# Optimization experiments

Measured on AMD Instinct MI355X. Metric: run time of the kernel, lower is better.

The kernel has to match this reference:

```python
import jax, jax.numpy as jnp
import numpy as np

K = 9      # kernel_size
H = 6      # num_head
HD = 64    # head_dim
D = H * HD # reduced_hidden_dim = 384
B, S = 16, 1024
OUT = 384  # hidden_dim // 2


def setup_inputs() -> dict:
    key = jax.random.key(0)
    k = jax.random.split(key, 5)
    q = jax.random.normal(k[0], (B, S, D), dtype=jnp.float32)
    ks = jax.random.normal(k[1], (B, S, D), dtype=jnp.float32)
    v = jax.random.normal(k[2], (B, S, D), dtype=jnp.float32)
    Wk = jax.random.normal(k[3], (K * H, D), dtype=jnp.float32) * 0.02
    bk = jnp.zeros((K * H,), dtype=jnp.float32)
    Wp = jax.random.normal(k[4], (OUT, D), dtype=jnp.float32) * 0.02
    bp = jnp.zeros((OUT,), dtype=jnp.float32)
    return {"q": q, "ks": ks, "v": v, "Wk": Wk, "bk": bk, "Wp": Wp, "bp": bp}


def reference(q, ks, v, Wk, bk, Wp, bp):
    b, s, d = v.shape
    pad = K // 2
    # expand4conv: zero-pad along seq and gather K-wide sliding windows
    vp = jnp.pad(v, ((0, 0), (pad, pad), (0, 0)))            # [B, S+K-1, D]
    win = jnp.stack([vp[:, i:i + s] for i in range(K)], -1)  # [B, S, D, K]
    win = win.reshape(b, s, H, HD, K)                        # [B, S, H, HD, K]
    # dynamic kernel: softmax over kernel taps
    logits = jnp.einsum('bsd,od->bso', q * ks, Wk) + bk       # [B, S, K*H]
    dk = jax.nn.softmax(logits.reshape(b, s, H, K), axis=-1)  # [B, S, H, K]
    # local weighted reduction over the window
    out = jnp.einsum('bshdk,bshk->bshd', win, dk).reshape(b, s, d)
    return jnp.einsum('bsd,od->bso', out, Wp) + bp            # [B, S, OUT]
```

## Files before the change

### kernel.cpp

```cpp
#include <hip/hip_runtime.h>
#include <hip/hip_bf16.h>

#define BB 16
#define SS 1024
#define DD 384
#define HH 6
#define HDD 64
#define KK 9
#define KH 54
#define NP 64
#define OUTD 384

typedef __attribute__((ext_vector_type(4))) float floatx4;
typedef __attribute__((ext_vector_type(8))) __bf16 bf16x8;
typedef __attribute__((ext_vector_type(4))) __bf16 bf16x4;

#define QLD 392
#define VLD 392

__global__ __launch_bounds__(256) void cast_kernel(const float* __restrict__ Wk,
                                                   const float* __restrict__ Wp,
                                                   __bf16* __restrict__ WkB,
                                                   __bf16* __restrict__ WpB) {
    int i = blockIdx.x * 256 + threadIdx.x;
    if (i < NP * DD) {
        int r = i / DD;
        WkB[i] = (r < KH) ? (__bf16)Wk[i] : (__bf16)0.0f;
    } else {
        int j = i - NP * DD;
        if (j < OUTD * DD) WpB[j] = (__bf16)Wp[j];
    }
}

__global__ __launch_bounds__(256) void fused_kernel(const float* __restrict__ q,
                                                    const float* __restrict__ ks,
                                                    const float* __restrict__ v,
                                                    const __bf16* __restrict__ WkB,
                                                    const float* __restrict__ bk,
                                                    __bf16* __restrict__ outA) {
    __shared__ __bf16 vqS[40 * VLD];
    __shared__ float  lgS[2 * 32 * 66];
    __shared__ float  dkS[32 * 56];

    const int tid  = threadIdx.x;
    const int wave = tid >> 6;
    const int lane = tid & 63;
    const int m0   = blockIdx.x * 32;
    const int b    = blockIdx.x >> 5;
    const int s0   = (blockIdx.x & 31) * 32;

    {
        const float* qb = q  + (size_t)m0 * DD;
        const float* kb = ks + (size_t)m0 * DD;
#pragma unroll
        for (int it = 0; it < 12; ++it) {
            int c = tid + it * 256;
            int row = c / 96, col = (c % 96) * 4;
            floatx4 qv = *reinterpret_cast<const floatx4*>(qb + (size_t)row * DD + col);
            floatx4 kv = *reinterpret_cast<const floatx4*>(kb + (size_t)row * DD + col);
            floatx4 pr = qv * kv;
            bf16x4 pk = { (__bf16)pr.x, (__bf16)pr.y, (__bf16)pr.z, (__bf16)pr.w };
            *reinterpret_cast<bf16x4*>(&vqS[row * VLD + col]) = pk;
        }
    }
    __syncthreads();

    {
        const int wm = (wave & 1) * 16;
        const int kh = wave >> 1;
        const int fr = lane & 15;
        const int fk = (lane >> 4) * 8;
        floatx4 acc[4] = {};
#pragma unroll
        for (int s = 0; s < 6; ++s) {
            int kk = kh * 192 + s * 32;
            bf16x8 afrag = *reinterpret_cast<const bf16x8*>(&vqS[(wm + fr) * VLD + kk + fk]);
#pragma unroll
            for (int j = 0; j < 4; ++j) {
                bf16x8 bfrag = *reinterpret_cast<const bf16x8*>(
                    WkB + (size_t)(j * 16 + fr) * DD + kk + fk);
                acc[j] = __builtin_amdgcn_mfma_f32_16x16x32_bf16(afrag, bfrag, acc[j], 0, 0, 0);
            }
        }
        const int col_in = lane & 15;
        const int rgrp   = (lane >> 4) * 4;
#pragma unroll
        for (int j = 0; j < 4; ++j)
#pragma unroll
            for (int r = 0; r < 4; ++r)
                lgS[(kh * 32 + wm + rgrp + r) * 66 + j * 16 + col_in] = acc[j][r];
    }
    __syncthreads();

    if (tid < 32 * HH) {
        int row = tid / HH, h = tid % HH;
        float lg[KK];
        float mx = -1e30f;
#pragma unroll
        for (int k = 0; k < KK; ++k) {
            int o = h * KK + k;
            float s = lgS[row * 66 + o] + lgS[(32 + row) * 66 + o] + bk[o];
            lg[k] = s;
            mx = fmaxf(mx, s);
        }
        float sum = 0.0f;
#pragma unroll
        for (int k = 0; k < KK; ++k) { lg[k] = __expf(lg[k] - mx); sum += lg[k]; }
        float inv = 1.0f / sum;
#pragma unroll
        for (int k = 0; k < KK; ++k) dkS[row * 56 + h * KK + k] = lg[k] * inv;
    }

    {
        const float* vb = v + (size_t)b * SS * DD;
#pragma unroll
        for (int it = 0; it < 15; ++it) {
            int c = tid + it * 256;
            int row = c / 96, col = (c % 96) * 4;
            int r = s0 + row - 4;
            floatx4 val = {};
            if (r >= 0 && r < SS)
                val = *reinterpret_cast<const floatx4*>(vb + (size_t)r * DD + col);
            bf16x4 vk = { (__bf16)val.x, (__bf16)val.y, (__bf16)val.z, (__bf16)val.w };
            *reinterpret_cast<bf16x4*>(&vqS[row * VLD + col]) = vk;
        }
    }
    __syncthreads();

    __bf16* ob = outA + (size_t)m0 * DD;
#pragma unroll
    for (int it = 0; it < 12; ++it) {
        int p = tid + it * 256;
        int row = p / 96, c4 = p % 96;
        int h = c4 >> 4;
        const float* dkr = &dkS[row * 56 + h * KK];
        floatx4 a = {};
#pragma unroll
        for (int k = 0; k < KK; ++k) {
            bf16x4 w = *reinterpret_cast<const bf16x4*>(&vqS[(row + k) * VLD + c4 * 4]);
            floatx4 wf = { (float)w[0], (float)w[1], (float)w[2], (float)w[3] };
            a += wf * dkr[k];
        }
        bf16x4 o = { (__bf16)a.x, (__bf16)a.y, (__bf16)a.z, (__bf16)a.w };
        *reinterpret_cast<bf16x4*>(&ob[(size_t)row * DD + c4 * 4]) = o;
    }
}

__global__ __launch_bounds__(256) void gemm_kernel(const __bf16* __restrict__ A,
                                                   const __bf16* __restrict__ Bw,
                                                   const float* __restrict__ bias,
                                                   float* __restrict__ Cout) {
    __shared__ __bf16 Bs[64 * QLD];

    const int tid  = threadIdx.x;
    const int wave = tid >> 6;
    const int lane = tid & 63;

    const int mtile = blockIdx.x / (OUTD / 64);
    const int ntile = blockIdx.x % (OUTD / 64);
    const int m0 = mtile * 128;
    const int n0 = ntile * 64;

#pragma unroll 4
    for (int j = 0; j < 12; ++j) {
        int id = tid + j * 256;
        int r = id / 48, ch = (id % 48) * 8;
        *reinterpret_cast<bf16x8*>(&Bs[r * QLD + ch]) =
            *reinterpret_cast<const bf16x8*>(Bw + (size_t)(n0 + r) * DD + ch);
    }
    __syncthreads();

    const int wm = wave * 32;
    const int fr = lane & 15;
    const int fk = (lane >> 4) * 8;

    floatx4 acc[2][4] = {};

#pragma unroll 4
    for (int kk = 0; kk < DD; kk += 32) {
        bf16x8 afrag[2];
#pragma unroll
        for (int i = 0; i < 2; ++i)
            afrag[i] = *reinterpret_cast<const bf16x8*>(
                A + (size_t)(m0 + wm + i * 16 + fr) * DD + kk + fk);
#pragma unroll
        for (int j = 0; j < 4; ++j) {
            bf16x8 bfrag = *reinterpret_cast<const bf16x8*>(&Bs[(j * 16 + fr) * QLD + kk + fk]);
#pragma unroll
            for (int i = 0; i < 2; ++i)
                acc[i][j] = __builtin_amdgcn_mfma_f32_16x16x32_bf16(afrag[i], bfrag, acc[i][j], 0, 0, 0);
        }
    }

    const int col_in = lane & 15;
    const int rgrp   = (lane >> 4) * 4;
#pragma unroll
    for (int i = 0; i < 2; ++i) {
#pragma unroll
        for (int j = 0; j < 4; ++j) {
            int col = n0 + j * 16 + col_in;
            float bv = bias[col];
#pragma unroll
            for (int r = 0; r < 4; ++r) {
                int row = m0 + wm + i * 16 + rgrp + r;
                Cout[(size_t)row * OUTD + col] = acc[i][j][r] + bv;
            }
        }
    }
}

extern "C" void kernel_launch(void* const* d_in, const int* in_sizes, int n_in,
                              void* d_out, int out_size, void* d_ws, size_t ws_size,
                              hipStream_t stream) {
    const float* q  = (const float*)d_in[0];
    const float* ks = (const float*)d_in[1];
    const float* v  = (const float*)d_in[2];
    const float* Wk = (const float*)d_in[3];
    const float* bk = (const float*)d_in[4];
    const float* Wp = (const float*)d_in[5];
    const float* bp = (const float*)d_in[6];
    float* out = (float*)d_out;

    __bf16* WpB = (__bf16*)d_ws;
    __bf16* WkB = (__bf16*)((char*)d_ws + 294912);
    __bf16* Abf = (__bf16*)((char*)d_ws + 294912 + 49152);

    cast_kernel<<<(NP * DD + OUTD * DD + 255) / 256, 256, 0, stream>>>(Wk, Wp, WkB, WpB);
    fused_kernel<<<(BB * SS) / 32, 256, 0, stream>>>(q, ks, v, WkB, bk, Abf);
    gemm_kernel<<<(BB * SS / 128) * (OUTD / 64), 256, 0, stream>>>(Abf, WpB, bp, out);
}
```

Measured before the change: 143.8 us.

## Fuse output projection GEMM into fused kernel with MFMA-fragment-ordered weights

The separate output-projection GEMM kernel is removed. Its work now runs at the end of the fused kernel: the bf16 windowed result stays in shared memory, a buffer that reuses the logits space, and feeds MFMA directly. The cast kernel now writes Wk and Wp in per-lane MFMA fragment order, so B fragments load as contiguous 16-byte chunks straight from global memory. This removes the intermediate activation round trip through HBM and one kernel launch. In exchange, each block rereads the whole Wp from L2, and each wave carries 12 accumulators.

```diff
diff --git a/kernel.cpp b/kernel.cpp
--- a/kernel.cpp
+++ b/kernel.cpp
@@ -5,42 +5,50 @@
 #define SS 1024
 #define DD 384
 #define HH 6
-#define HDD 64
 #define KK 9
 #define KH 54
-#define NP 64
 #define OUTD 384
+#define NKT 12
+#define VLD 392
 
 typedef __attribute__((ext_vector_type(4))) float floatx4;
 typedef __attribute__((ext_vector_type(8))) __bf16 bf16x8;
 typedef __attribute__((ext_vector_type(4))) __bf16 bf16x4;
 
-#define QLD 392
-#define VLD 392
-
 __global__ __launch_bounds__(256) void cast_kernel(const float* __restrict__ Wk,
                                                    const float* __restrict__ Wp,
-                                                   __bf16* __restrict__ WkB,
-                                                   __bf16* __restrict__ WpB) {
+                                                   __bf16* __restrict__ WkT,
+                                                   __bf16* __restrict__ WpT) {
     int i = blockIdx.x * 256 + threadIdx.x;
-    if (i < NP * DD) {
-        int r = i / DD;
-        WkB[i] = (r < KH) ? (__bf16)Wk[i] : (__bf16)0.0f;
-    } else {
-        int j = i - NP * DD;
-        if (j < OUTD * DD) WpB[j] = (__bf16)Wp[j];
+    if (i < 4 * NKT * 64 * 8) {
+        int e = i & 7, lane = (i >> 3) & 63, t = i >> 9;
+        int kstep = t % NKT, ntile = t / NKT;
+        int row = ntile * 16 + (lane & 15);
+        int col = kstep * 32 + ((lane >> 4) << 3) + e;
+        WkT[i] = (row < KH) ? (__bf16)Wk[row * DD + col] : (__bf16)0.0f;
+    } else if (i < 24576 + 24 * NKT * 64 * 8) {
+        int j = i - 24576;
+        int e = j & 7, lane = (j >> 3) & 63, t = j >> 9;
+        int kstep = t % NKT, ntile = t / NKT;
+        int row = ntile * 16 + (lane & 15);
+        int col = kstep * 32 + ((lane >> 4) << 3) + e;
+        WpT[j] = (__bf16)Wp[row * DD + col];
     }
 }
 
 __global__ __launch_bounds__(256) void fused_kernel(const float* __restrict__ q,
                                                     const float* __restrict__ ks,
                                                     const float* __restrict__ v,
-                                                    const __bf16* __restrict__ WkB,
+                                                    const __bf16* __restrict__ WkT,
                                                     const float* __restrict__ bk,
-                                                    __bf16* __restrict__ outA) {
+                                                    const __bf16* __restrict__ WpT,
+                                                    const float* __restrict__ bp,
+                                                    float* __restrict__ out) {
     __shared__ __bf16 vqS[40 * VLD];
-    __shared__ float  lgS[2 * 32 * 66];
     __shared__ float  dkS[32 * 56];
+    __shared__ __align__(16) char uS[32 * VLD * 2];
+    float*  lgS = (float*)uS;
+    __bf16* aS  = (__bf16*)uS;
 
     const int tid  = threadIdx.x;
     const int wave = tid >> 6;
@@ -48,6 +56,10 @@
     const int m0   = blockIdx.x * 32;
     const int b    = blockIdx.x >> 5;
     const int s0   = (blockIdx.x & 31) * 32;
+    const int fr   = lane & 15;
+    const int fk   = (lane >> 4) * 8;
+    const int col_in = lane & 15;
+    const int rgrp   = (lane >> 4) * 4;
 
     {
         const float* qb = q  + (size_t)m0 * DD;
@@ -66,29 +78,25 @@
     __syncthreads();
 
     {
-        const int wm = (wave & 1) * 16;
-        const int kh = wave >> 1;
-        const int fr = lane & 15;
-        const int fk = (lane >> 4) * 8;
+        const int wml = (wave & 1) * 16;
+        const int kh  = wave >> 1;
         floatx4 acc[4] = {};
 #pragma unroll
         for (int s = 0; s < 6; ++s) {
-            int kk = kh * 192 + s * 32;
-            bf16x8 afrag = *reinterpret_cast<const bf16x8*>(&vqS[(wm + fr) * VLD + kk + fk]);
+            int kst = kh * 6 + s;
+            bf16x8 af = *reinterpret_cast<const bf16x8*>(&vqS[(wml + fr) * VLD + kst * 32 + fk]);
 #pragma unroll
             for (int j = 0; j < 4; ++j) {
-                bf16x8 bfrag = *reinterpret_cast<const bf16x8*>(
-                    WkB + (size_t)(j * 16 + fr) * DD + kk + fk);
-                acc[j] = __builtin_amdgcn_mfma_f32_16x16x32_bf16(afrag, bfrag, acc[j], 0, 0, 0);
+                bf16x8 bf = *reinterpret_cast<const bf16x8*>(
+                    WkT + (((j * NKT + kst) * 64 + lane) << 3));
+                acc[j] = __builtin_amdgcn_mfma_f32_16x16x32_bf16(af, bf, acc[j], 0, 0, 0);
             }
         }
-        const int col_in = lane & 15;
-        const int rgrp   = (lane >> 4) * 4;
 #pragma unroll
         for (int j = 0; j < 4; ++j)
 #pragma unroll
             for (int r = 0; r < 4; ++r)
-                lgS[(kh * 32 + wm + rgrp + r) * 66 + j * 16 + col_in] = acc[j][r];
+                lgS[(kh * 32 + wml + rgrp + r) * 66 + j * 16 + col_in] = acc[j][r];
     }
     __syncthreads();
 
@@ -110,7 +118,6 @@
 #pragma unroll
         for (int k = 0; k < KK; ++k) dkS[row * 56 + h * KK + k] = lg[k] * inv;
     }
-
     {
         const float* vb = v + (size_t)b * SS * DD;
 #pragma unroll
@@ -127,7 +134,6 @@
     }
     __syncthreads();
 
-    __bf16* ob = outA + (size_t)m0 * DD;
 #pragma unroll
     for (int it = 0; it < 12; ++it) {
         int p = tid + it * 256;
@@ -142,69 +148,32 @@
             a += wf * dkr[k];
         }
         bf16x4 o = { (__bf16)a.x, (__bf16)a.y, (__bf16)a.z, (__bf16)a.w };
-        *reinterpret_cast<bf16x4*>(&ob[(size_t)row * DD + c4 * 4]) = o;
-    }
-}
-
-__global__ __launch_bounds__(256) void gemm_kernel(const __bf16* __restrict__ A,
-                                                   const __bf16* __restrict__ Bw,
-                                                   const float* __restrict__ bias,
-                                                   float* __restrict__ Cout) {
-    __shared__ __bf16 Bs[64 * QLD];
-
-    const int tid  = threadIdx.x;
-    const int wave = tid >> 6;
-    const int lane = tid & 63;
-
-    const int mtile = blockIdx.x / (OUTD / 64);
-    const int ntile = blockIdx.x % (OUTD / 64);
-    const int m0 = mtile * 128;
-    const int n0 = ntile * 64;
-
-#pragma unroll 4
-    for (int j = 0; j < 12; ++j) {
-        int id = tid + j * 256;
-        int r = id / 48, ch = (id % 48) * 8;
-        *reinterpret_cast<bf16x8*>(&Bs[r * QLD + ch]) =
-            *reinterpret_cast<const bf16x8*>(Bw + (size_t)(n0 + r) * DD + ch);
+        *reinterpret_cast<bf16x4*>(&aS[row * VLD + c4 * 4]) = o;
     }
     __syncthreads();
 
-    const int wm = wave * 32;
-    const int fr = lane & 15;
-    const int fk = (lane >> 4) * 8;
-
-    floatx4 acc[2][4] = {};
-
-#pragma unroll 4
-    for (int kk = 0; kk < DD; kk += 32) {
-        bf16x8 afrag[2];
+    {
+        const int wm  = (wave & 1) * 16;
+        const int nt0 = (wave >> 1) * 12;
+        floatx4 acc[12] = {};
+#pragma unroll 2
+        for (int s = 0; s < NKT; ++s) {
+            bf16x8 af = *reinterpret_cast<const bf16x8*>(&aS[(wm + fr) * VLD + s * 32 + fk]);
 #pragma unroll
-        for (int i = 0; i < 2; ++i)
-            afrag[i] = *reinterpret_cast<const bf16x8*>(
-                A + (size_t)(m0 + wm + i * 16 + fr) * DD + kk + fk);
+            for (int j = 0; j < 12; ++j) {
+                bf16x8 bf = *reinterpret_cast<const bf16x8*>(
+                    WpT + ((((nt0 + j) * NKT + s) * 64 + lane) << 3));
+                acc[j] = __builtin_amdgcn_mfma_f32_16x16x32_bf16(af, bf, acc[j], 0, 0, 0);
+            }
+        }
+        float* ob = out + (size_t)m0 * OUTD;
 #pragma unroll
-        for (int j = 0; j < 4; ++j) {
-            bf16x8 bfrag = *reinterpret_cast<const bf16x8*>(&Bs[(j * 16 + fr) * QLD + kk + fk]);
+        for (int j = 0; j < 12; ++j) {
+            int col = (nt0 + j) * 16 + col_in;
+            float bv = bp[col];
 #pragma unroll
-            for (int i = 0; i < 2; ++i)
-                acc[i][j] = __builtin_amdgcn_mfma_f32_16x16x32_bf16(afrag[i], bfrag, acc[i][j], 0, 0, 0);
-        }
-    }
-
-    const int col_in = lane & 15;
-    const int rgrp   = (lane >> 4) * 4;
-#pragma unroll
-    for (int i = 0; i < 2; ++i) {
-#pragma unroll
-        for (int j = 0; j < 4; ++j) {
-            int col = n0 + j * 16 + col_in;
-            float bv = bias[col];
-#pragma unroll
-            for (int r = 0; r < 4; ++r) {
-                int row = m0 + wm + i * 16 + rgrp + r;
-                Cout[(size_t)row * OUTD + col] = acc[i][j][r] + bv;
-            }
+            for (int r = 0; r < 4; ++r)
+                ob[(size_t)(wm + rgrp + r) * OUTD + col] = acc[j][r] + bv;
         }
     }
 }
@@ -221,11 +190,9 @@
     const float* bp = (const float*)d_in[6];
     float* out = (float*)d_out;
 
-    __bf16* WpB = (__bf16*)d_ws;
-    __bf16* WkB = (__bf16*)((char*)d_ws + 294912);
-    __bf16* Abf = (__bf16*)((char*)d_ws + 294912 + 49152);
+    __bf16* WkT = (__bf16*)d_ws;
+    __bf16* WpT = (__bf16*)((char*)d_ws + 49152);
 
-    cast_kernel<<<(NP * DD + OUTD * DD + 255) / 256, 256, 0, stream>>>(Wk, Wp, WkB, WpB);
-    fused_kernel<<<(BB * SS) / 32, 256, 0, stream>>>(q, ks, v, WkB, bk, Abf);
-    gemm_kernel<<<(BB * SS / 128) * (OUTD / 64), 256, 0, stream>>>(Abf, WpB, bp, out);
+    cast_kernel<<<(24576 + 147456 + 255) / 256, 256, 0, stream>>>(Wk, Wp, WkT, WpT);
+    fused_kernel<<<(BB * SS) / 32, 256, 0, stream>>>(q, ks, v, WkT, bk, WpT, bp, out);
 }
```

After: 130.1 us. 9.5% less time.
